# Kernel optimization log

Hardware: AMD Instinct MI355X
Metric: run time of the kernel (lower is better)

Reference implementation:

```python
import jax, jax.numpy as jnp
import numpy as np

BS, C, H, W = 4, 128, 64, 64  # input_dim=128
INNER = 64


def setup_inputs() -> dict:
    key = jax.random.key(0)
    ks = jax.random.split(key, 9)
    s_in = 1.0 / np.sqrt(C)
    s_inner = 1.0 / np.sqrt(INNER)
    return {
        "inpt": jax.random.normal(ks[0], (BS, C, H, W), dtype=jnp.float32),
        "Wq": jax.random.normal(ks[1], (INNER, C), dtype=jnp.float32) * s_in,
        "bq": jax.random.normal(ks[2], (INNER,), dtype=jnp.float32) * 0.01,
        "Wk": jax.random.normal(ks[3], (INNER, C), dtype=jnp.float32) * s_in,
        "bk": jax.random.normal(ks[4], (INNER,), dtype=jnp.float32) * 0.01,
        "Wv": jax.random.normal(ks[5], (INNER, C), dtype=jnp.float32) * s_in,
        "bv": jax.random.normal(ks[6], (INNER,), dtype=jnp.float32) * 0.01,
        "Wo": jax.random.normal(ks[7], (C, INNER), dtype=jnp.float32) * s_inner,
        "bo": jax.random.normal(ks[8], (C,), dtype=jnp.float32) * 0.01,
    }


def reference(inpt, Wq, bq, Wk, bk, Wv, bv, Wo, bo):
    bs, c, h, w = inpt.shape
    L = h * w
    # [bs, C, H, W] -> [bs, L, C] (tokens = spatial positions)
    x = inpt.reshape(bs, c, L).transpose(0, 2, 1)
    q = jnp.einsum('blc,dc->bld', x, Wq) + bq  # [bs, L, INNER]
    k = jnp.einsum('blc,dc->bld', x, Wk) + bk
    v = jnp.einsum('blc,dc->bld', x, Wv) + bv
    # torch code divides by np.round(sqrt(d), 2); for d=64 this is exactly 8.0
    scale = jnp.float32(np.round(np.sqrt(q.shape[-1]), 2))
    scores = jnp.einsum('bld,bmd->blm', q, k) / scale  # [bs, L, L] score matrix
    factors = jax.nn.softmax(scores, axis=-1)
    ctx = jnp.einsum('blm,bmd->bld', factors, v)  # [bs, L, INNER]
    out = jnp.einsum('bld,cd->blc', ctx, Wo) + bo  # [bs, L, C]
    out = out.transpose(0, 2, 1).reshape(bs, c, h, w)
    return inpt + out
```

## Files before the change

kernel.cpp:

```cpp
#include <hip/hip_runtime.h>
#include <hip/hip_bf16.h>

typedef __bf16 bf16x8 __attribute__((ext_vector_type(8)));
typedef __bf16 bf16x4 __attribute__((ext_vector_type(4)));
typedef short  s16x4  __attribute__((ext_vector_type(4)));
typedef float  f32x4  __attribute__((ext_vector_type(4)));

#define MFMA32(a, b, c) __builtin_amdgcn_mfma_f32_16x16x32_bf16((a), (b), (c), 0, 0, 0)
#define MFMA16K(a, b, c) __builtin_amdgcn_mfma_f32_16x16x16bf16_1k((a), (b), (c), 0, 0, 0)

#if __has_builtin(__builtin_amdgcn_exp2f)
#define EXP2F(x) __builtin_amdgcn_exp2f(x)
#else
#define EXP2F(x) __expf(0.6931471805599453f * (x))
#endif

#define GL16(G, L)                                                            \
    __builtin_amdgcn_global_load_lds(                                         \
        (const __attribute__((address_space(1))) void*)(G),                   \
        (__attribute__((address_space(3))) void*)(L), 16, 0, 0)

#define SPLIT 4
#define QSCALE 0.18033688011112042f

__global__ __launch_bounds__(256) void qkv_kernel(
    const float* __restrict__ inpt,
    const float* __restrict__ Wq, const float* __restrict__ bq,
    const float* __restrict__ Wk, const float* __restrict__ bk,
    const float* __restrict__ Wv, const float* __restrict__ bv,
    __bf16* __restrict__ Qws, __bf16* __restrict__ Kws, __bf16* __restrict__ VTws)
{
    __shared__ __align__(16) __bf16 xT[16 * 140];
    const int bid = blockIdx.x;
    const int b   = bid >> 8;
    const int l0  = (bid & 255) << 4;
    const int t   = threadIdx.x;

    {
        const int c = t >> 1, half = t & 1;
        const float* xin = inpt + ((size_t)(b * 128 + c)) * 4096 + l0 + half * 8;
        float4 v0 = *(const float4*)xin;
        float4 v1 = *(const float4*)(xin + 4);
        const int tok0 = half * 8;
        xT[(tok0 + 0) * 140 + c] = (__bf16)v0.x;
        xT[(tok0 + 1) * 140 + c] = (__bf16)v0.y;
        xT[(tok0 + 2) * 140 + c] = (__bf16)v0.z;
        xT[(tok0 + 3) * 140 + c] = (__bf16)v0.w;
        xT[(tok0 + 4) * 140 + c] = (__bf16)v1.x;
        xT[(tok0 + 5) * 140 + c] = (__bf16)v1.y;
        xT[(tok0 + 6) * 140 + c] = (__bf16)v1.z;
        xT[(tok0 + 7) * 140 + c] = (__bf16)v1.w;
    }
    __syncthreads();

    const int w    = t >> 6;
    const int lane = t & 63;
    const int quad = lane >> 4;
    const int l15  = lane & 15;

    f32x4 acc[3];
    #pragma unroll
    for (int j = 0; j < 3; ++j)
        #pragma unroll
        for (int r = 0; r < 4; ++r) acc[j][r] = 0.f;

    #pragma unroll
    for (int ks = 0; ks < 4; ++ks) {
        bf16x8 af = *(const bf16x8*)&xT[l15 * 140 + ks * 32 + quad * 8];
        #pragma unroll
        for (int j = 0; j < 3; ++j) {
            const int wn   = w * 3 + j;
            const int msel = wn >> 2;
            const float* W = (msel == 0) ? Wq : ((msel == 1) ? Wk : Wv);
            const float* Wp = W + ((wn & 3) * 16 + l15) * 128 + ks * 32 + quad * 8;
            float4 wa = *(const float4*)Wp;
            float4 wb = *(const float4*)(Wp + 4);
            bf16x8 bf;
            bf[0] = (__bf16)wa.x; bf[1] = (__bf16)wa.y;
            bf[2] = (__bf16)wa.z; bf[3] = (__bf16)wa.w;
            bf[4] = (__bf16)wb.x; bf[5] = (__bf16)wb.y;
            bf[6] = (__bf16)wb.z; bf[7] = (__bf16)wb.w;
            acc[j] = MFMA32(af, bf, acc[j]);
        }
    }

    #pragma unroll
    for (int j = 0; j < 3; ++j) {
        const int wn   = w * 3 + j;
        const int msel = wn >> 2;
        const int o0   = (wn & 3) * 16;
        const float* bb = (msel == 0) ? bq : ((msel == 1) ? bk : bv);
        float bias = bb[o0 + l15];
        if (msel < 2) {
            __bf16* base = (msel == 0) ? Qws : Kws;
            const float scl = (msel == 0) ? QSCALE : 1.0f;
            #pragma unroll
            for (int r = 0; r < 4; ++r) {
                float v = (acc[j][r] + bias) * scl;
                base[((size_t)(b * 4096 + l0 + quad * 4 + r)) * 64 + o0 + l15] = (__bf16)v;
            }
        } else {
            const int d = o0 + l15;
            #pragma unroll
            for (int r = 0; r < 4; ++r) {
                float v = acc[j][r] + bias;
                VTws[((size_t)(b * 64 + d)) * 4096 + l0 + quad * 4 + r] = (__bf16)v;
            }
        }
    }
}

__global__ __launch_bounds__(256, 4) void attn_kernel(
    const __bf16* __restrict__ Qws, const __bf16* __restrict__ Kws,
    const __bf16* __restrict__ VTws,
    float* __restrict__ Ops, float* __restrict__ Mws, float* __restrict__ Lws)
{
    __shared__ __align__(16) __bf16 sbuf[2][8192];

    const int bid   = blockIdx.x;
    const int split = bid >> 8;
    const int qt    = bid & 255;
    const int b  = qt >> 6;
    const int l0 = (qt & 63) << 6;
    const int t    = threadIdx.x;
    const int w    = t >> 6;
    const int lane = t & 63;
    const int quad = lane >> 4;
    const int l15  = lane & 15;
    const int l7   = l15 & 7;

    const __bf16* qptr = Qws + ((size_t)(b * 4096 + l0 + w * 16 + l15)) * 64 + quad * 8;
    bf16x8 qf0 = *(const bf16x8*)qptr;
    bf16x8 qf1 = *(const bf16x8*)(qptr + 32);

    f32x4 cfr[4];
    #pragma unroll
    for (int mt = 0; mt < 4; ++mt)
        #pragma unroll
        for (int r = 0; r < 4; ++r) cfr[mt][r] = 0.f;
    float m_run = -1e30f, l_run = 0.f;

    const uint4* Kg = (const uint4*)(Kws + ((size_t)b << 18));
    const uint4* Vg = (const uint4*)(VTws + ((size_t)b << 18));
    const int rw = t >> 3, cw = (t & 7) ^ ((t >> 3) & 7);
    const uint4* kp = Kg + rw * 8 + cw + split * 8192;
    const uint4* vp = Vg + (size_t)rw * 512 + cw + split * 128;

    union B4 { bf16x4 h; s16x4 s; };

    {
        __bf16* Bb = sbuf[0];
        GL16(kp,         Bb +        w * 512);
        GL16(kp + 256,   Bb + 2048 + w * 512);
        GL16(vp,         Bb + 4096 + w * 512);
        GL16(vp + 16384, Bb + 6144 + w * 512);
        kp += 512; vp += 8;
    }

    for (int kt = 0; kt < 16; ++kt) {
        const int cur = kt & 1;
        __syncthreads();
        if (kt < 15) {
            __bf16* Bb = sbuf[cur ^ 1];
            GL16(kp,         Bb +        w * 512);
            GL16(kp + 256,   Bb + 2048 + w * 512);
            GL16(vp,         Bb + 4096 + w * 512);
            GL16(vp + 16384, Bb + 6144 + w * 512);
            kp += 512; vp += 8;
        }
        const __bf16* B = sbuf[cur];

        f32x4 s[4];
        #pragma unroll
        for (int nt = 0; nt < 4; ++nt) {
            const int key = nt * 16 + l15;
            const int sw  = key * 8;
            const int kx  = key & 7;
            bf16x8 kf0 = *(const bf16x8*)&B[(sw + (quad ^ kx)) * 8];
            bf16x8 kf1 = *(const bf16x8*)&B[(sw + ((quad + 4) ^ kx)) * 8];
            f32x4 a = {0.f, 0.f, 0.f, 0.f};
            a = MFMA32(kf0, qf0, a);
            a = MFMA32(kf1, qf1, a);
            s[nt] = a;
        }

        float mx = -1e30f;
        #pragma unroll
        for (int nt = 0; nt < 4; ++nt)
            #pragma unroll
            for (int r = 0; r < 4; ++r) mx = fmaxf(mx, s[nt][r]);
        mx = fmaxf(mx, __shfl_xor(mx, 16));
        mx = fmaxf(mx, __shfl_xor(mx, 32));
        float mnew  = fmaxf(m_run, mx);
        float alpha = EXP2F(m_run - mnew);
        m_run = mnew;

        float psum = 0.f;
        B4 pk[4];
        #pragma unroll
        for (int nt = 0; nt < 4; ++nt) {
            #pragma unroll
            for (int r = 0; r < 4; ++r) {
                float p = EXP2F(s[nt][r] - mnew);
                psum += p;
                pk[nt].h[r] = (__bf16)p;
            }
        }
        psum += __shfl_xor(psum, 16);
        psum += __shfl_xor(psum, 32);
        l_run = l_run * alpha + psum;

        #pragma unroll
        for (int mt = 0; mt < 4; ++mt)
            #pragma unroll
            for (int r = 0; r < 4; ++r) cfr[mt][r] *= alpha;

        const __bf16* Vb = B + 4096;
        const int q2 = quad >> 1, q1 = (quad & 1) * 4;
        #pragma unroll
        for (int kc = 0; kc < 4; ++kc) {
            #pragma unroll
            for (int mt = 0; mt < 4; ++mt) {
                const int d  = mt * 16 + l15;
                const int cc = (2 * kc + q2) ^ l7;
                B4 vf;
                vf.h = *(const bf16x4*)&Vb[(d * 8 + cc) * 8 + q1];
                cfr[mt] = MFMA16K(vf.s, pk[kc].s, cfr[mt]);
            }
        }
    }

    const int l   = l0 + w * 16 + l15;
    const int row = (split * 4 + b) * 4096 + l;
    float* obase = Ops + (size_t)row * 64;
    #pragma unroll
    for (int mt = 0; mt < 4; ++mt)
        *(f32x4*)(obase + mt * 16 + quad * 4) = cfr[mt];
    if (quad == 0) { Mws[row] = m_run; Lws[row] = l_run; }
}

__global__ __launch_bounds__(256) void outproj_kernel(
    const float* __restrict__ inpt,
    const float* __restrict__ Ops, const float* __restrict__ Mws,
    const float* __restrict__ Lws,
    const float* __restrict__ Wo, const float* __restrict__ bo,
    float* __restrict__ out)
{
    __shared__ __align__(16) __bf16 cx[16 * 72];
    const int bid = blockIdx.x;
    const int b   = bid >> 8;
    const int l0  = (bid & 255) << 4;
    const int t   = threadIdx.x;

    {
        const int token = t >> 4, d4 = (t & 15) << 2;
        const int rowb  = b * 4096 + l0 + token;
        float m[SPLIT], ls[SPLIT], gmax = -1e30f;
        #pragma unroll
        for (int s = 0; s < SPLIT; ++s) {
            const int ro = s * 16384 + rowb;
            m[s] = Mws[ro]; ls[s] = Lws[ro];
            gmax = fmaxf(gmax, m[s]);
        }
        float denom = 0.f, e[SPLIT];
        #pragma unroll
        for (int s = 0; s < SPLIT; ++s) { e[s] = EXP2F(m[s] - gmax); denom += e[s] * ls[s]; }
        const float inv = 1.f / denom;
        float ax = 0.f, ay = 0.f, az = 0.f, aw = 0.f;
        #pragma unroll
        for (int s = 0; s < SPLIT; ++s) {
            const float4 v = *(const float4*)(Ops + ((size_t)(s * 16384 + rowb)) * 64 + d4);
            const float wgt = e[s] * inv;
            ax += wgt * v.x; ay += wgt * v.y; az += wgt * v.z; aw += wgt * v.w;
        }
        bf16x4 pv;
        pv[0] = (__bf16)ax; pv[1] = (__bf16)ay; pv[2] = (__bf16)az; pv[3] = (__bf16)aw;
        *(bf16x4*)&cx[token * 72 + d4] = pv;
    }
    __syncthreads();

    const int w    = t >> 6;
    const int lane = t & 63;
    const int quad = lane >> 4;
    const int l15  = lane & 15;

    f32x4 acc[2];
    #pragma unroll
    for (int mi = 0; mi < 2; ++mi)
        #pragma unroll
        for (int r = 0; r < 4; ++r) acc[mi][r] = 0.f;

    #pragma unroll
    for (int ks = 0; ks < 2; ++ks) {
        bf16x8 bfrag = *(const bf16x8*)&cx[l15 * 72 + ks * 32 + quad * 8];
        #pragma unroll
        for (int mi = 0; mi < 2; ++mi) {
            const int crow = (w * 2 + mi) * 16 + l15;
            const float* Wp = Wo + crow * 64 + ks * 32 + quad * 8;
            float4 wa = *(const float4*)Wp;
            float4 wb = *(const float4*)(Wp + 4);
            bf16x8 afrag;
            afrag[0] = (__bf16)wa.x; afrag[1] = (__bf16)wa.y;
            afrag[2] = (__bf16)wa.z; afrag[3] = (__bf16)wa.w;
            afrag[4] = (__bf16)wb.x; afrag[5] = (__bf16)wb.y;
            afrag[6] = (__bf16)wb.z; afrag[7] = (__bf16)wb.w;
            acc[mi] = MFMA32(afrag, bfrag, acc[mi]);
        }
    }

    #pragma unroll
    for (int mi = 0; mi < 2; ++mi) {
        #pragma unroll
        for (int r = 0; r < 4; ++r) {
            const int c = (w * 2 + mi) * 16 + quad * 4 + r;
            const size_t addr = ((size_t)(b * 128 + c)) * 4096 + l0 + l15;
            out[addr] = inpt[addr] + bo[c] + acc[mi][r];
        }
    }
}

extern "C" void kernel_launch(void* const* d_in, const int* in_sizes, int n_in,
                              void* d_out, int out_size, void* d_ws, size_t ws_size,
                              hipStream_t stream)
{
    const float* inpt = (const float*)d_in[0];
    const float* Wq   = (const float*)d_in[1];
    const float* bq   = (const float*)d_in[2];
    const float* Wk   = (const float*)d_in[3];
    const float* bk   = (const float*)d_in[4];
    const float* Wv   = (const float*)d_in[5];
    const float* bv   = (const float*)d_in[6];
    const float* Wo   = (const float*)d_in[7];
    const float* bo   = (const float*)d_in[8];
    float* out = (float*)d_out;

    char* ws = (char*)d_ws;
    const size_t MB = (size_t)1 << 20;
    __bf16* Qws  = (__bf16*)(ws + 0 * MB);
    __bf16* Kws  = (__bf16*)(ws + 2 * MB);
    __bf16* VTws = (__bf16*)(ws + 4 * MB);
    float*  Ops  = (float*)(ws + 6 * MB);
    float*  Mws  = (float*)(ws + 22 * MB);
    float*  Lws  = (float*)(ws + 22 * MB + 256 * 1024);

    qkv_kernel<<<1024, 256, 0, stream>>>(inpt, Wq, bq, Wk, bk, Wv, bv, Qws, Kws, VTws);
    attn_kernel<<<SPLIT * 256, 256, 0, stream>>>(Qws, Kws, VTws, Ops, Mws, Lws);
    outproj_kernel<<<1024, 256, 0, stream>>>(inpt, Ops, Mws, Lws, Wo, bo, out);
}
```

Measured before the change: 134.1 us.

## Double query rows per attention block, raise split-K to 8, stage QK stores via LDS

Each attention wave now handles two 16-row query tiles instead of one, so every K/V tile loaded into LDS feeds twice as many MFMAs. The key dimension is split into 8 chunks instead of 4 to keep the grid at 1024 blocks, which doubles the partial-output workspace and the merge work in outproj. The qkv kernel also stages Q/K results in shared memory so it can write them back as 16-byte coalesced stores, and writes V^T with 8-byte vector stores. The cost is higher register pressure in attn_kernel and more partial-result traffic to reduce.

```diff
diff --git a/kernel.cpp b/kernel.cpp
--- a/kernel.cpp
+++ b/kernel.cpp
@@ -20,7 +20,7 @@
         (const __attribute__((address_space(1))) void*)(G),                   \
         (__attribute__((address_space(3))) void*)(L), 16, 0, 0)
 
-#define SPLIT 4
+#define SPLIT 8
 #define QSCALE 0.18033688011112042f
 
 __global__ __launch_bounds__(256) void qkv_kernel(
@@ -31,6 +31,7 @@
     __bf16* __restrict__ Qws, __bf16* __restrict__ Kws, __bf16* __restrict__ VTws)
 {
     __shared__ __align__(16) __bf16 xT[16 * 140];
+    __shared__ __align__(16) __bf16 os[16 * 144];
     const int bid = blockIdx.x;
     const int b   = bid >> 8;
     const int l0  = (bid & 255) << 4;
@@ -92,21 +93,28 @@
         const float* bb = (msel == 0) ? bq : ((msel == 1) ? bk : bv);
         float bias = bb[o0 + l15];
         if (msel < 2) {
-            __bf16* base = (msel == 0) ? Qws : Kws;
             const float scl = (msel == 0) ? QSCALE : 1.0f;
-            #pragma unroll
-            for (int r = 0; r < 4; ++r) {
-                float v = (acc[j][r] + bias) * scl;
-                base[((size_t)(b * 4096 + l0 + quad * 4 + r)) * 64 + o0 + l15] = (__bf16)v;
-            }
+            const int oc = wn * 16 + l15;
+            #pragma unroll
+            for (int r = 0; r < 4; ++r)
+                os[(quad * 4 + r) * 144 + oc] = (__bf16)((acc[j][r] + bias) * scl);
         } else {
             const int d = o0 + l15;
-            #pragma unroll
-            for (int r = 0; r < 4; ++r) {
-                float v = acc[j][r] + bias;
-                VTws[((size_t)(b * 64 + d)) * 4096 + l0 + quad * 4 + r] = (__bf16)v;
-            }
-        }
+            bf16x4 v;
+            #pragma unroll
+            for (int r = 0; r < 4; ++r) v[r] = (__bf16)(acc[j][r] + bias);
+            *(bf16x4*)(VTws + ((size_t)(b * 64 + d)) * 4096 + l0 + quad * 4) = v;
+        }
+    }
+    __syncthreads();
+
+    {
+        const int tok = t >> 4, c = t & 15;
+        bf16x8 v = *(const bf16x8*)&os[tok * 144 + c * 8];
+        __bf16* dst = (c < 8)
+            ? Qws + ((size_t)(b * 4096 + l0 + tok)) * 64 + c * 8
+            : Kws + ((size_t)(b * 4096 + l0 + tok)) * 64 + (c - 8) * 8;
+        *(bf16x8*)dst = v;
     }
 }
 
@@ -118,10 +126,10 @@
     __shared__ __align__(16) __bf16 sbuf[2][8192];
 
     const int bid   = blockIdx.x;
-    const int split = bid >> 8;
-    const int qt    = bid & 255;
-    const int b  = qt >> 6;
-    const int l0 = (qt & 63) << 6;
+    const int split = bid >> 7;
+    const int rest  = bid & 127;
+    const int b   = rest >> 5;
+    const int l0  = (rest & 31) << 7;
     const int t    = threadIdx.x;
     const int w    = t >> 6;
     const int lane = t & 63;
@@ -129,22 +137,29 @@
     const int l15  = lane & 15;
     const int l7   = l15 & 7;
 
-    const __bf16* qptr = Qws + ((size_t)(b * 4096 + l0 + w * 16 + l15)) * 64 + quad * 8;
-    bf16x8 qf0 = *(const bf16x8*)qptr;
-    bf16x8 qf1 = *(const bf16x8*)(qptr + 32);
-
-    f32x4 cfr[4];
-    #pragma unroll
-    for (int mt = 0; mt < 4; ++mt)
-        #pragma unroll
-        for (int r = 0; r < 4; ++r) cfr[mt][r] = 0.f;
-    float m_run = -1e30f, l_run = 0.f;
+    bf16x8 qf[2][2];
+    #pragma unroll
+    for (int u = 0; u < 2; ++u) {
+        const __bf16* qptr = Qws
+            + ((size_t)(b * 4096 + l0 + w * 32 + u * 16 + l15)) * 64 + quad * 8;
+        qf[u][0] = *(const bf16x8*)qptr;
+        qf[u][1] = *(const bf16x8*)(qptr + 32);
+    }
+
+    f32x4 cfr[2][4];
+    #pragma unroll
+    for (int u = 0; u < 2; ++u)
+        #pragma unroll
+        for (int mt = 0; mt < 4; ++mt)
+            #pragma unroll
+            for (int r = 0; r < 4; ++r) cfr[u][mt][r] = 0.f;
+    float m_run[2] = {-1e30f, -1e30f}, l_run[2] = {0.f, 0.f};
 
     const uint4* Kg = (const uint4*)(Kws + ((size_t)b << 18));
     const uint4* Vg = (const uint4*)(VTws + ((size_t)b << 18));
     const int rw = t >> 3, cw = (t & 7) ^ ((t >> 3) & 7);
-    const uint4* kp = Kg + rw * 8 + cw + split * 8192;
-    const uint4* vp = Vg + (size_t)rw * 512 + cw + split * 128;
+    const uint4* kp = Kg + rw * 8 + cw + split * 4096;
+    const uint4* vp = Vg + (size_t)rw * 512 + cw + split * 64;
 
     union B4 { bf16x4 h; s16x4 s; };
 
@@ -157,10 +172,10 @@
         kp += 512; vp += 8;
     }
 
-    for (int kt = 0; kt < 16; ++kt) {
+    for (int kt = 0; kt < 8; ++kt) {
         const int cur = kt & 1;
         __syncthreads();
-        if (kt < 15) {
+        if (kt < 7) {
             __bf16* Bb = sbuf[cur ^ 1];
             GL16(kp,         Bb +        w * 512);
             GL16(kp + 256,   Bb + 2048 + w * 512);
@@ -170,7 +185,7 @@
         }
         const __bf16* B = sbuf[cur];
 
-        f32x4 s[4];
+        f32x4 s[2][4];
         #pragma unroll
         for (int nt = 0; nt < 4; ++nt) {
             const int key = nt * 16 + l15;
@@ -178,42 +193,48 @@
             const int kx  = key & 7;
             bf16x8 kf0 = *(const bf16x8*)&B[(sw + (quad ^ kx)) * 8];
             bf16x8 kf1 = *(const bf16x8*)&B[(sw + ((quad + 4) ^ kx)) * 8];
-            f32x4 a = {0.f, 0.f, 0.f, 0.f};
-            a = MFMA32(kf0, qf0, a);
-            a = MFMA32(kf1, qf1, a);
-            s[nt] = a;
-        }
-
-        float mx = -1e30f;
-        #pragma unroll
-        for (int nt = 0; nt < 4; ++nt)
-            #pragma unroll
-            for (int r = 0; r < 4; ++r) mx = fmaxf(mx, s[nt][r]);
-        mx = fmaxf(mx, __shfl_xor(mx, 16));
-        mx = fmaxf(mx, __shfl_xor(mx, 32));
-        float mnew  = fmaxf(m_run, mx);
-        float alpha = EXP2F(m_run - mnew);
-        m_run = mnew;
-
-        float psum = 0.f;
-        B4 pk[4];
-        #pragma unroll
-        for (int nt = 0; nt < 4; ++nt) {
-            #pragma unroll
-            for (int r = 0; r < 4; ++r) {
-                float p = EXP2F(s[nt][r] - mnew);
-                psum += p;
-                pk[nt].h[r] = (__bf16)p;
+            #pragma unroll
+            for (int u = 0; u < 2; ++u) {
+                f32x4 a = {0.f, 0.f, 0.f, 0.f};
+                a = MFMA32(kf0, qf[u][0], a);
+                a = MFMA32(kf1, qf[u][1], a);
+                s[u][nt] = a;
             }
         }
-        psum += __shfl_xor(psum, 16);
-        psum += __shfl_xor(psum, 32);
-        l_run = l_run * alpha + psum;
-
-        #pragma unroll
-        for (int mt = 0; mt < 4; ++mt)
-            #pragma unroll
-            for (int r = 0; r < 4; ++r) cfr[mt][r] *= alpha;
+
+        B4 pk[2][4];
+        #pragma unroll
+        for (int u = 0; u < 2; ++u) {
+            float mx = -1e30f;
+            #pragma unroll
+            for (int nt = 0; nt < 4; ++nt)
+                #pragma unroll
+                for (int r = 0; r < 4; ++r) mx = fmaxf(mx, s[u][nt][r]);
+            mx = fmaxf(mx, __shfl_xor(mx, 16));
+            mx = fmaxf(mx, __shfl_xor(mx, 32));
+            float mnew  = fmaxf(m_run[u], mx);
+            float alpha = EXP2F(m_run[u] - mnew);
+            m_run[u] = mnew;
+
+            float psum = 0.f;
+            #pragma unroll
+            for (int nt = 0; nt < 4; ++nt) {
+                #pragma unroll
+                for (int r = 0; r < 4; ++r) {
+                    float p = EXP2F(s[u][nt][r] - mnew);
+                    psum += p;
+                    pk[u][nt].h[r] = (__bf16)p;
+                }
+            }
+            psum += __shfl_xor(psum, 16);
+            psum += __shfl_xor(psum, 32);
+            l_run[u] = l_run[u] * alpha + psum;
+
+            #pragma unroll
+            for (int mt = 0; mt < 4; ++mt)
+                #pragma unroll
+                for (int r = 0; r < 4; ++r) cfr[u][mt][r] *= alpha;
+        }
 
         const __bf16* Vb = B + 4096;
         const int q2 = quad >> 1, q1 = (quad & 1) * 4;
@@ -225,18 +246,22 @@
                 const int cc = (2 * kc + q2) ^ l7;
                 B4 vf;
                 vf.h = *(const bf16x4*)&Vb[(d * 8 + cc) * 8 + q1];
-                cfr[mt] = MFMA16K(vf.s, pk[kc].s, cfr[mt]);
+                cfr[0][mt] = MFMA16K(vf.s, pk[0][kc].s, cfr[0][mt]);
+                cfr[1][mt] = MFMA16K(vf.s, pk[1][kc].s, cfr[1][mt]);
             }
         }
     }
 
-    const int l   = l0 + w * 16 + l15;
-    const int row = (split * 4 + b) * 4096 + l;
-    float* obase = Ops + (size_t)row * 64;
-    #pragma unroll
-    for (int mt = 0; mt < 4; ++mt)
-        *(f32x4*)(obase + mt * 16 + quad * 4) = cfr[mt];
-    if (quad == 0) { Mws[row] = m_run; Lws[row] = l_run; }
+    #pragma unroll
+    for (int u = 0; u < 2; ++u) {
+        const int l   = l0 + w * 32 + u * 16 + l15;
+        const int row = (split * 4 + b) * 4096 + l;
+        float* obase = Ops + (size_t)row * 64;
+        #pragma unroll
+        for (int mt = 0; mt < 4; ++mt)
+            *(f32x4*)(obase + mt * 16 + quad * 4) = cfr[u][mt];
+        if (quad == 0) { Mws[row] = m_run[u]; Lws[row] = l_run[u]; }
+    }
 }
 
 __global__ __launch_bounds__(256) void outproj_kernel(
@@ -340,10 +365,10 @@
     __bf16* Kws  = (__bf16*)(ws + 2 * MB);
     __bf16* VTws = (__bf16*)(ws + 4 * MB);
     float*  Ops  = (float*)(ws + 6 * MB);
-    float*  Mws  = (float*)(ws + 22 * MB);
-    float*  Lws  = (float*)(ws + 22 * MB + 256 * 1024);
+    float*  Mws  = (float*)(ws + 38 * MB);
+    float*  Lws  = (float*)(ws + 39 * MB);
 
     qkv_kernel<<<1024, 256, 0, stream>>>(inpt, Wq, bq, Wk, bk, Wv, bv, Qws, Kws, VTws);
-    attn_kernel<<<SPLIT * 256, 256, 0, stream>>>(Qws, Kws, VTws, Ops, Mws, Lws);
+    attn_kernel<<<SPLIT * 128, 256, 0, stream>>>(Qws, Kws, VTws, Ops, Mws, Lws);
     outproj_kernel<<<1024, 256, 0, stream>>>(inpt, Ops, Mws, Lws, Wo, bo, out);
 }
```

Result: slower. 139.5 us (+4.0%).
